# Kernel tuning notes

Hardware: AMD Instinct MI355X
Metric: run time of the kernel (lower is better)

The kernel has to match this reference:

```python
import jax, jax.numpy as jnp
import numpy as np

SIGMA = 0.5          # cone height of the distance field
B, NV, NF, MAXC = 32, 6890, 13776, 8
NC = NF * MAXC       # padded number of collision pair slots


def setup_inputs() -> dict:
    key = jax.random.key(0)
    ks = jax.random.split(key, 8)
    return {
        "pose": jax.random.normal(ks[0], (B, 72), jnp.float32),
        "joints": jax.random.normal(ks[1], (B, 24, 3), jnp.float32),
        "points": jax.random.normal(ks[2], (B, 118, 3), jnp.float32),
        "keypoints": jax.random.normal(ks[3], (B, 118, 3), jnp.float32),
        "vertices": jax.random.normal(ks[4], (B, NV, 3), jnp.float32),
        "weight": jnp.ones((1,), jnp.float32),
        "faces": jax.random.randint(ks[5], (NF, 3), 0, NV, dtype=jnp.int32),
        "collision_idxs": jax.random.randint(ks[6], (B, NC, 2), 0, NF, dtype=jnp.int32),
    }


def _cone_point2plane(cone_tris, query_tris):
    """Conic distance-field penetration (point2plane), vectorized over pairs.
    cone_tris/query_tris: [B, C, 3 verts, 3 xyz]. Returns [B, C]."""
    c = cone_tris.mean(axis=-2)                              # centroid [B,C,3]
    e1 = cone_tris[..., 1, :] - cone_tris[..., 0, :]
    e2 = cone_tris[..., 2, :] - cone_tris[..., 0, :]
    n = jnp.cross(e1, e2)
    n = n / (jnp.linalg.norm(n, axis=-1, keepdims=True) + 1e-8)
    d = query_tris - c[..., None, :]                         # [B,C,3,3]
    h = jnp.einsum('bcvk,bck->bcv', d, n)                    # signed plane dist
    r = jnp.linalg.norm(d, axis=-1)                          # dist to centroid
    phi = jnp.maximum(SIGMA - r, 0.0)                        # linear cone field
    pen = jnp.where(h < 0, phi * h * h, 0.0)                 # penetrating verts only
    return pen.sum(axis=-1)


def reference(pose, joints, points, keypoints, vertices, weight, faces, collision_idxs):
    # polygons = verts.view(-1,3)[faces_idx]  ->  per-batch face gather
    tris = jnp.take(vertices, faces, axis=1)                 # [B,NF,3,3]
    recv_idx = collision_idxs[..., 0]
    intr_idx = collision_idxs[..., 1]
    valid = recv_idx >= 0                                    # -1 padding slots

    def gather(idx):
        idx = jnp.maximum(idx, 0)[:, :, None, None]
        return jnp.take_along_axis(tris, idx, axis=1)        # [B,NC,3,3]

    recv = gather(recv_idx)
    intr = gather(intr_idx)
    # symmetric penetration: intruder verts in receiver's field and vice versa
    pen = _cone_point2plane(recv, intr) + _cone_point2plane(intr, recv)
    loss = jnp.where(valid, pen, 0.0).sum() / B
    return loss * weight[0]
```

## Files before the change

### kernel.cpp

```cpp
#include <hip/hip_runtime.h>

#define SIGMA 0.5f
#define BB 32
#define NVV 6890
#define NFF 13776
#define MAXC 8
#define NCC (NFF * MAXC)

#define SLOTS 8
#define PAIRS_PER_SLOT (NCC / SLOTS)
#define THREADS 1024
#define NBLOCK (BB * SLOTS)

typedef int v4i __attribute__((ext_vector_type(4)));

__device__ __forceinline__ float3 loadv3(const float* __restrict__ p) {
    return make_float3(p[0], p[1], p[2]);
}

__device__ __forceinline__ float conePen(float3 a0, float3 a1, float3 a2,
                                         float3 q0, float3 q1, float3 q2) {
    const float third = 1.0f / 3.0f;
    float cx = (a0.x + a1.x + a2.x) * third;
    float cy = (a0.y + a1.y + a2.y) * third;
    float cz = (a0.z + a1.z + a2.z) * third;
    float e1x = a1.x - a0.x, e1y = a1.y - a0.y, e1z = a1.z - a0.z;
    float e2x = a2.x - a0.x, e2y = a2.y - a0.y, e2z = a2.z - a0.z;
    float nx = e1y * e2z - e1z * e2y;
    float ny = e1z * e2x - e1x * e2z;
    float nz = e1x * e2y - e1y * e2x;
    float inv = 1.0f / (sqrtf(nx * nx + ny * ny + nz * nz) + 1e-8f);
    nx *= inv; ny *= inv; nz *= inv;
    float3 q[3] = {q0, q1, q2};
    float pen = 0.0f;
#pragma unroll
    for (int v = 0; v < 3; ++v) {
        float dx = q[v].x - cx, dy = q[v].y - cy, dz = q[v].z - cz;
        float h = dx * nx + dy * ny + dz * nz;
        float r = sqrtf(dx * dx + dy * dy + dz * dz);
        float phi = fmaxf(SIGMA - r, 0.0f);
        pen += (h < 0.0f) ? phi * h * h : 0.0f;
    }
    return pen;
}

__device__ __forceinline__ float3 ldsVert(const float* __restrict__ sv, int v) {
    return make_float3(sv[3 * v + 0], sv[3 * v + 1], sv[3 * v + 2]);
}

__device__ __forceinline__ float pairPen(const float* __restrict__ sv,
                                         const unsigned int* __restrict__ fw,
                                         const unsigned char* __restrict__ fb,
                                         int r, int it) {
    if (r < 0) return 0.0f;
    const int g = it < 0 ? 0 : it;
    unsigned int wa = fw[r];
    unsigned int wb = fw[g];
    int a0 = wa & 8191, a1 = (wa >> 13) & 8191, a2 = (int)(wa >> 26) | ((int)fb[r] << 6);
    int b0 = wb & 8191, b1 = (wb >> 13) & 8191, b2 = (int)(wb >> 26) | ((int)fb[g] << 6);
    float3 A0 = ldsVert(sv, a0), A1 = ldsVert(sv, a1), A2 = ldsVert(sv, a2);
    float3 B0 = ldsVert(sv, b0), B1 = ldsVert(sv, b1), B2 = ldsVert(sv, b2);
    return conePen(A0, A1, A2, B0, B1, B2) + conePen(B0, B1, B2, A0, A1, A2);
}

__global__ __launch_bounds__(THREADS) void fused_kernel(
    const float* __restrict__ vertices,
    const int*   __restrict__ faces,
    const int*   __restrict__ cidx,
    float*       __restrict__ partials)
{
    __shared__ float         s_v[NVV * 3];
    __shared__ unsigned int  s_fw[NFF];
    __shared__ unsigned char s_fb[NFF];
    __shared__ float         s_red[16];

    const int b   = blockIdx.x;
    const int sl  = blockIdx.y;
    const int tid = threadIdx.x;

    const float* vb = vertices + (size_t)b * (NVV * 3);
    for (int i = tid; i < NVV * 3; i += THREADS)
        s_v[i] = vb[i];

    for (int f = tid; f < NFF; f += THREADS) {
        int i0 = faces[3 * f + 0];
        int i1 = faces[3 * f + 1];
        int i2 = faces[3 * f + 2];
        s_fw[f] = (unsigned int)i0 | ((unsigned int)i1 << 13)
                | ((unsigned int)(i2 & 63) << 26);
        s_fb[f] = (unsigned char)(i2 >> 6);
    }
    __syncthreads();

    float pen = 0.0f;
    const v4i* c4 = (const v4i*)(cidx + ((size_t)b * NCC + (size_t)sl * PAIRS_PER_SLOT) * 2);
    for (int q = tid; 2 * q < PAIRS_PER_SLOT; q += THREADS) {
        v4i pr = __builtin_nontemporal_load(c4 + q);
        pen += pairPen(s_v, s_fw, s_fb, pr.x, pr.y);
        pen += pairPen(s_v, s_fw, s_fb, pr.z, pr.w);
    }

#pragma unroll
    for (int off = 32; off > 0; off >>= 1)
        pen += __shfl_down(pen, off, 64);
    const int lane = tid & 63;
    const int wv   = tid >> 6;
    if (lane == 0) s_red[wv] = pen;
    __syncthreads();
    if (tid == 0) {
        float t = 0.0f;
#pragma unroll
        for (int w = 0; w < 16; ++w) t += s_red[w];
        partials[b * SLOTS + sl] = t;
    }
}

__global__ __launch_bounds__(256) void fin2_kernel(
    const float* __restrict__ partials,
    const float* __restrict__ weight,
    float*       __restrict__ out)
{
    float s = partials[threadIdx.x];
#pragma unroll
    for (int off = 32; off > 0; off >>= 1)
        s += __shfl_down(s, off, 64);
    __shared__ float smem[4];
    const int lane = threadIdx.x & 63;
    const int wv   = threadIdx.x >> 6;
    if (lane == 0) smem[wv] = s;
    __syncthreads();
    if (threadIdx.x == 0)
        out[0] = (smem[0] + smem[1] + smem[2] + smem[3]) * weight[0] * (1.0f / (float)BB);
}

__global__ void init_kernel(float* __restrict__ accum) { accum[0] = 0.0f; }

__global__ __launch_bounds__(256) void pen_direct(
    const float* __restrict__ vertices, const int* __restrict__ faces,
    const int2* __restrict__ cidx, float* __restrict__ accum)
{
    const int i = blockIdx.x * blockDim.x + threadIdx.x;
    float pen = 0.0f;
    if (i < BB * NCC) {
        const int b = i / NCC;
        const int2 pr = cidx[i];
        if (pr.x >= 0) {
            const int f0 = pr.x;
            const int f1 = pr.y < 0 ? 0 : pr.y;
            const float* vb = vertices + (size_t)b * (NVV * 3);
            float3 a0 = loadv3(vb + (size_t)faces[f0*3+0] * 3);
            float3 a1 = loadv3(vb + (size_t)faces[f0*3+1] * 3);
            float3 a2 = loadv3(vb + (size_t)faces[f0*3+2] * 3);
            float3 b0 = loadv3(vb + (size_t)faces[f1*3+0] * 3);
            float3 b1 = loadv3(vb + (size_t)faces[f1*3+1] * 3);
            float3 b2 = loadv3(vb + (size_t)faces[f1*3+2] * 3);
            pen = conePen(a0,a1,a2,b0,b1,b2) + conePen(b0,b1,b2,a0,a1,a2);
        }
    }
#pragma unroll
    for (int off = 32; off > 0; off >>= 1)
        pen += __shfl_down(pen, off, 64);
    __shared__ float smem[4];
    const int lane = threadIdx.x & 63;
    const int wv   = threadIdx.x >> 6;
    if (lane == 0) smem[wv] = pen;
    __syncthreads();
    if (threadIdx.x == 0)
        atomicAdd(accum, smem[0] + smem[1] + smem[2] + smem[3]);
}

__global__ void fin_kernel(const float* __restrict__ accum,
                           const float* __restrict__ weight,
                           float* __restrict__ out)
{
    out[0] = accum[0] * weight[0] * (1.0f / (float)BB);
}

extern "C" void kernel_launch(void* const* d_in, const int* in_sizes, int n_in,
                              void* d_out, int out_size, void* d_ws, size_t ws_size,
                              hipStream_t stream) {
    const float* vertices = (const float*)d_in[4];
    const float* weight   = (const float*)d_in[5];
    const int*   faces    = (const int*)d_in[6];
    const int*   cidx     = (const int*)d_in[7];
    float* out = (float*)d_out;

    if (ws_size >= NBLOCK * sizeof(float)) {
        float* partials = (float*)d_ws;
        fused_kernel<<<dim3(BB, SLOTS), dim3(THREADS), 0, stream>>>(
            vertices, faces, cidx, partials);
        fin2_kernel<<<dim3(1), dim3(256), 0, stream>>>(partials, weight, out);
    } else {
        float* accum = (float*)d_ws;
        const int totalPairs = BB * NCC;
        init_kernel<<<dim3(1), dim3(1), 0, stream>>>(accum);
        pen_direct<<<dim3((totalPairs + 255) / 256), dim3(256), 0, stream>>>(
            vertices, faces, (const int2*)cidx, accum);
        fin_kernel<<<dim3(1), dim3(1), 0, stream>>>(accum, weight, out);
    }
}
```

Baseline: 123.7 us.

## Store vertices as fp16 in LDS with byte-offset face indices and 2x unrolled pair loop

Vertices are converted to half precision and packed as 8-byte h4 entries in shared memory, so each vertex is fetched with a single LDS load instead of three float loads. Face indices are stored pre-scaled as byte offsets in a 16+16-bit word plus a ushort, which removes the bit unpacking. The pair loop now handles two index vectors per iteration to increase memory-level parallelism. The fp16 storage loses precision in the distance computations and could change the loss beyond tolerance.

```diff
diff --git a/kernel.cpp b/kernel.cpp
--- a/kernel.cpp
+++ b/kernel.cpp
@@ -9,10 +9,12 @@
 
 #define SLOTS 8
 #define PAIRS_PER_SLOT (NCC / SLOTS)
+#define QHALF (PAIRS_PER_SLOT / 4)
 #define THREADS 1024
 #define NBLOCK (BB * SLOTS)
 
-typedef int v4i __attribute__((ext_vector_type(4)));
+typedef int       v4i __attribute__((ext_vector_type(4)));
+typedef _Float16  h4  __attribute__((ext_vector_type(4)));
 
 __device__ __forceinline__ float3 loadv3(const float* __restrict__ p) {
     return make_float3(p[0], p[1], p[2]);
@@ -44,22 +46,27 @@
     return pen;
 }
 
-__device__ __forceinline__ float3 ldsVert(const float* __restrict__ sv, int v) {
-    return make_float3(sv[3 * v + 0], sv[3 * v + 1], sv[3 * v + 2]);
-}
-
-__device__ __forceinline__ float pairPen(const float* __restrict__ sv,
-                                         const unsigned int* __restrict__ fw,
-                                         const unsigned char* __restrict__ fb,
+__device__ __forceinline__ float3 ldsVertB(const h4* __restrict__ sv, unsigned int boff) {
+    h4 h = *(const h4*)((const char*)sv + boff);
+    return make_float3((float)h.x, (float)h.y, (float)h.z);
+}
+
+__device__ __forceinline__ float pairPen(const h4* __restrict__ sv,
+                                         const unsigned int*   __restrict__ f01,
+                                         const unsigned short* __restrict__ f2,
                                          int r, int it) {
     if (r < 0) return 0.0f;
     const int g = it < 0 ? 0 : it;
-    unsigned int wa = fw[r];
-    unsigned int wb = fw[g];
-    int a0 = wa & 8191, a1 = (wa >> 13) & 8191, a2 = (int)(wa >> 26) | ((int)fb[r] << 6);
-    int b0 = wb & 8191, b1 = (wb >> 13) & 8191, b2 = (int)(wb >> 26) | ((int)fb[g] << 6);
-    float3 A0 = ldsVert(sv, a0), A1 = ldsVert(sv, a1), A2 = ldsVert(sv, a2);
-    float3 B0 = ldsVert(sv, b0), B1 = ldsVert(sv, b1), B2 = ldsVert(sv, b2);
+    unsigned int wa = f01[r];
+    unsigned int wb = f01[g];
+    unsigned int oa2 = f2[r];
+    unsigned int ob2 = f2[g];
+    float3 A0 = ldsVertB(sv, wa & 0xFFFFu);
+    float3 A1 = ldsVertB(sv, wa >> 16);
+    float3 A2 = ldsVertB(sv, oa2);
+    float3 B0 = ldsVertB(sv, wb & 0xFFFFu);
+    float3 B1 = ldsVertB(sv, wb >> 16);
+    float3 B2 = ldsVertB(sv, ob2);
     return conePen(A0, A1, A2, B0, B1, B2) + conePen(B0, B1, B2, A0, A1, A2);
 }
 
@@ -69,35 +76,44 @@
     const int*   __restrict__ cidx,
     float*       __restrict__ partials)
 {
-    __shared__ float         s_v[NVV * 3];
-    __shared__ unsigned int  s_fw[NFF];
-    __shared__ unsigned char s_fb[NFF];
-    __shared__ float         s_red[16];
+    __shared__ h4             s_v[NVV];
+    __shared__ unsigned int   s_f01[NFF];
+    __shared__ unsigned short s_f2[NFF];
+    __shared__ float          s_red[16];
 
     const int b   = blockIdx.x;
     const int sl  = blockIdx.y;
     const int tid = threadIdx.x;
 
     const float* vb = vertices + (size_t)b * (NVV * 3);
-    for (int i = tid; i < NVV * 3; i += THREADS)
-        s_v[i] = vb[i];
+    for (int v = tid; v < NVV; v += THREADS) {
+        const float* p = vb + 3 * v;
+        h4 h;
+        h.x = (_Float16)p[0];
+        h.y = (_Float16)p[1];
+        h.z = (_Float16)p[2];
+        h.w = (_Float16)0.0f;
+        s_v[v] = h;
+    }
 
     for (int f = tid; f < NFF; f += THREADS) {
         int i0 = faces[3 * f + 0];
         int i1 = faces[3 * f + 1];
         int i2 = faces[3 * f + 2];
-        s_fw[f] = (unsigned int)i0 | ((unsigned int)i1 << 13)
-                | ((unsigned int)(i2 & 63) << 26);
-        s_fb[f] = (unsigned char)(i2 >> 6);
+        s_f01[f] = (unsigned int)(i0 << 3) | ((unsigned int)(i1 << 3) << 16);
+        s_f2[f]  = (unsigned short)(i2 << 3);
     }
     __syncthreads();
 
     float pen = 0.0f;
     const v4i* c4 = (const v4i*)(cidx + ((size_t)b * NCC + (size_t)sl * PAIRS_PER_SLOT) * 2);
-    for (int q = tid; 2 * q < PAIRS_PER_SLOT; q += THREADS) {
-        v4i pr = __builtin_nontemporal_load(c4 + q);
-        pen += pairPen(s_v, s_fw, s_fb, pr.x, pr.y);
-        pen += pairPen(s_v, s_fw, s_fb, pr.z, pr.w);
+    for (int q = tid; q < QHALF; q += THREADS) {
+        v4i pA = __builtin_nontemporal_load(c4 + q);
+        v4i pB = __builtin_nontemporal_load(c4 + q + QHALF);
+        pen += pairPen(s_v, s_f01, s_f2, pA.x, pA.y);
+        pen += pairPen(s_v, s_f01, s_f2, pA.z, pA.w);
+        pen += pairPen(s_v, s_f01, s_f2, pB.x, pB.y);
+        pen += pairPen(s_v, s_f01, s_f2, pB.z, pB.w);
     }
 
 #pragma unroll
```

New measurement: 126.1 us. About the same (+1.9%).
